# Kernel tuning notes

Measured on AMD Instinct MI355X. Metric: run time of the kernel, lower is better.

## Reference

```python
import jax, jax.numpy as jnp
import numpy as np

COST_CLASS, COST_BBOX, COST_GIOU = 1.0, 5.0, 2.0


def box_cxcywh_to_xyxy(x):
    cx, cy, w, h = x[..., 0], x[..., 1], x[..., 2], x[..., 3]
    return jnp.stack([cx - 0.5 * w, cy - 0.5 * h, cx + 0.5 * w, cy + 0.5 * h], axis=-1)


def generalized_box_iou(boxes1, boxes2):
    # boxes1: [M,4] xyxy, boxes2: [T,4] xyxy -> [M,T]
    area1 = (boxes1[:, 2] - boxes1[:, 0]) * (boxes1[:, 3] - boxes1[:, 1])
    area2 = (boxes2[:, 2] - boxes2[:, 0]) * (boxes2[:, 3] - boxes2[:, 1])
    lt = jnp.maximum(boxes1[:, None, :2], boxes2[None, :, :2])
    rb = jnp.minimum(boxes1[:, None, 2:], boxes2[None, :, 2:])
    wh = jnp.clip(rb - lt, 0.0)
    inter = wh[:, :, 0] * wh[:, :, 1]
    union = area1[:, None] + area2[None, :] - inter
    iou = inter / union
    lt_e = jnp.minimum(boxes1[:, None, :2], boxes2[None, :, :2])
    rb_e = jnp.maximum(boxes1[:, None, 2:], boxes2[None, :, 2:])
    wh_e = jnp.clip(rb_e - lt_e, 0.0)
    area = wh_e[:, :, 0] * wh_e[:, :, 1]
    return iou - (area - union) / area


def setup_inputs() -> dict:
    key = jax.random.key(0)
    k1, k2, k3, k4 = jax.random.split(key, 4)
    B, Q, C, T = 32, 900, 92, 2048
    pred_logits = jax.random.normal(k1, (B, Q, C), dtype=jnp.float32)
    pred_boxes = jax.random.uniform(k2, (B, Q, 4), dtype=jnp.float32, minval=0.05, maxval=0.95)
    tgt_labels = jax.random.randint(k3, (T,), 0, C)
    tgt_boxes = jax.random.uniform(k4, (T, 4), dtype=jnp.float32, minval=0.05, maxval=0.95)
    return {"pred_logits": pred_logits, "pred_boxes": pred_boxes,
            "tgt_labels": tgt_labels, "tgt_boxes": tgt_boxes}


def reference(pred_logits, pred_boxes, tgt_labels, tgt_boxes):
    B, Q, C = pred_logits.shape
    out_prob = jax.nn.softmax(pred_logits.reshape(B * Q, C), axis=-1)  # [BQ, C]
    out_bbox = pred_boxes.reshape(B * Q, 4)                            # [BQ, 4]
    cost_class = -out_prob[:, tgt_labels]                              # [BQ, T] gather
    cost_bbox = jnp.sum(jnp.abs(out_bbox[:, None, :] - tgt_boxes[None, :, :]), axis=-1)  # L1 cdist
    cost_giou = -generalized_box_iou(box_cxcywh_to_xyxy(out_bbox), box_cxcywh_to_xyxy(tgt_boxes))
    Cmat = COST_CLASS * cost_class + COST_BBOX * cost_bbox + COST_GIOU * cost_giou
    return Cmat.reshape(B, Q, -1)
```

## Files before the change

kernel.cpp:

```cpp
#include <hip/hip_runtime.h>
#include <math.h>

#define NCLS 92
#define NTGT 2048

__global__ __launch_bounds__(256) void matcher_cost_kernel(
    const float* __restrict__ logits,
    const float* __restrict__ pboxes,
    const int*   __restrict__ tlabels,
    const float* __restrict__ tboxes,
    float* __restrict__ out)
{
    const int row  = blockIdx.x;
    const int tid  = threadIdx.x;
    const int lane = tid & 63;

    __shared__ float s_prob[NCLS];

    const float* lrow = logits + (long)row * NCLS;
    float v0 = lrow[lane];
    float v1 = (lane + 64 < NCLS) ? lrow[lane + 64] : -INFINITY;
    float m = fmaxf(v0, v1);
    #pragma unroll
    for (int s = 32; s >= 1; s >>= 1) m = fmaxf(m, __shfl_xor(m, s, 64));
    float e0 = expf(v0 - m);
    float e1 = (lane + 64 < NCLS) ? expf(v1 - m) : 0.0f;
    float ssum = e0 + e1;
    #pragma unroll
    for (int s = 32; s >= 1; s >>= 1) ssum += __shfl_xor(ssum, s, 64);
    const float rs = 1.0f / ssum;
    if (tid < 64) {
        s_prob[lane] = e0 * rs;
        if (lane + 64 < NCLS) s_prob[lane + 64] = e1 * rs;
    }

    const float4 pb = *(const float4*)(pboxes + (long)row * 4);
    const float pcx = pb.x, pcy = pb.y, pw = pb.z, ph = pb.w;
    const float px0 = pcx - 0.5f * pw, py0 = pcy - 0.5f * ph;
    const float px1 = pcx + 0.5f * pw, py1 = pcy + 0.5f * ph;
    const float parea = (px1 - px0) * (py1 - py0);

    __syncthreads();

    float* orow = out + (long)row * NTGT;

    #pragma unroll
    for (int pass = 0; pass < 2; ++pass) {
        const int t = pass * 1024 + tid * 4;
        const int4 lab = *(const int4*)(tlabels + t);
        float c[4];
        #pragma unroll
        for (int j = 0; j < 4; ++j) {
            const float4 tb = *(const float4*)(tboxes + (long)(t + j) * 4);
            const float tcx = tb.x, tcy = tb.y, tw = tb.z, th = tb.w;
            const float tx0 = tcx - 0.5f * tw, ty0 = tcy - 0.5f * th;
            const float tx1 = tcx + 0.5f * tw, ty1 = tcy + 0.5f * th;
            const float tarea = (tx1 - tx0) * (ty1 - ty0);

            const int labj = (j == 0) ? lab.x : (j == 1) ? lab.y : (j == 2) ? lab.z : lab.w;
            const float cc = -s_prob[labj];

            const float cb = fabsf(pcx - tcx) + fabsf(pcy - tcy)
                           + fabsf(pw  - tw ) + fabsf(ph  - th );

            const float xl = fmaxf(px0, tx0), yt = fmaxf(py0, ty0);
            const float xr = fminf(px1, tx1), yb = fminf(py1, ty1);
            const float iw = fmaxf(xr - xl, 0.0f), ih = fmaxf(yb - yt, 0.0f);
            const float inter = iw * ih;
            const float uni = parea + tarea - inter;
            const float iou = __fdividef(inter, uni);
            const float ex0 = fminf(px0, tx0), ey0 = fminf(py0, ty0);
            const float ex1 = fmaxf(px1, tx1), ey1 = fmaxf(py1, ty1);
            const float ew = fmaxf(ex1 - ex0, 0.0f), eh = fmaxf(ey1 - ey0, 0.0f);
            const float earea = ew * eh;
            const float giou = iou - __fdividef(earea - uni, earea);

            c[j] = cc + 5.0f * cb - 2.0f * giou;
        }
        *(float4*)(orow + t) = make_float4(c[0], c[1], c[2], c[3]);
    }
}

extern "C" void kernel_launch(void* const* d_in, const int* in_sizes, int n_in,
                              void* d_out, int out_size, void* d_ws, size_t ws_size,
                              hipStream_t stream) {
    const float* logits  = (const float*)d_in[0];
    const float* pboxes  = (const float*)d_in[1];
    const int*   tlabels = (const int*)  d_in[2];
    const float* tboxes  = (const float*)d_in[3];
    float* out = (float*)d_out;

    const int BQ = in_sizes[1] / 4;
    matcher_cost_kernel<<<BQ, 256, 0, stream>>>(logits, pboxes, tlabels, tboxes, out);
}
```

Before: 302.7 us.

## Process sixteen query rows per block and reuse target boxes in registers

Each block now handles 16 prediction rows instead of one. Sixteen-lane groups compute the softmax for each row in parallel into shared memory. Target boxes and labels are loaded once per thread and reused across all rows, which cuts redundant global loads and per-block setup overhead. Output uses nontemporal vector stores to reduce cache pollution, and each thread keeps more values live in registers.

Result: no change. 298.6 us (-1.4%).

```diff
diff --git a/kernel.cpp b/kernel.cpp
--- a/kernel.cpp
+++ b/kernel.cpp
@@ -3,81 +3,118 @@
 
 #define NCLS 92
 #define NTGT 2048
+#define ROWS 16
+
+typedef float vfloat4 __attribute__((ext_vector_type(4)));
 
 __global__ __launch_bounds__(256) void matcher_cost_kernel(
     const float* __restrict__ logits,
     const float* __restrict__ pboxes,
     const int*   __restrict__ tlabels,
     const float* __restrict__ tboxes,
-    float* __restrict__ out)
+    float* __restrict__ out,
+    int BQ)
 {
-    const int row  = blockIdx.x;
+    const int row0 = blockIdx.x * ROWS;
     const int tid  = threadIdx.x;
-    const int lane = tid & 63;
+    const int rlim = min(ROWS, BQ - row0);
 
-    __shared__ float s_prob[NCLS];
+    __shared__ float s_prob[ROWS][NCLS + 1];
+    __shared__ float s_pb[ROWS][12];
 
-    const float* lrow = logits + (long)row * NCLS;
-    float v0 = lrow[lane];
-    float v1 = (lane + 64 < NCLS) ? lrow[lane + 64] : -INFINITY;
-    float m = fmaxf(v0, v1);
-    #pragma unroll
-    for (int s = 32; s >= 1; s >>= 1) m = fmaxf(m, __shfl_xor(m, s, 64));
-    float e0 = expf(v0 - m);
-    float e1 = (lane + 64 < NCLS) ? expf(v1 - m) : 0.0f;
-    float ssum = e0 + e1;
-    #pragma unroll
-    for (int s = 32; s >= 1; s >>= 1) ssum += __shfl_xor(ssum, s, 64);
-    const float rs = 1.0f / ssum;
-    if (tid < 64) {
-        s_prob[lane] = e0 * rs;
-        if (lane + 64 < NCLS) s_prob[lane + 64] = e1 * rs;
+    {
+        const int g = tid >> 4;
+        const int l = tid & 15;
+        const int gr = (g < rlim) ? g : 0;
+        const float* lrow = logits + (long)(row0 + gr) * NCLS;
+        float v[6];
+        float m = -INFINITY;
+        #pragma unroll
+        for (int k = 0; k < 6; ++k) {
+            const int c = l + k * 16;
+            v[k] = (c < NCLS) ? lrow[c] : -INFINITY;
+            m = fmaxf(m, v[k]);
+        }
+        #pragma unroll
+        for (int s = 8; s >= 1; s >>= 1) m = fmaxf(m, __shfl_xor(m, s, 16));
+        float sum = 0.0f;
+        #pragma unroll
+        for (int k = 0; k < 6; ++k) {
+            const int c = l + k * 16;
+            v[k] = (c < NCLS) ? expf(v[k] - m) : 0.0f;
+            sum += v[k];
+        }
+        #pragma unroll
+        for (int s = 8; s >= 1; s >>= 1) sum += __shfl_xor(sum, s, 16);
+        const float rs = 1.0f / sum;
+        #pragma unroll
+        for (int k = 0; k < 6; ++k) {
+            const int c = l + k * 16;
+            if (c < NCLS) s_prob[g][c] = v[k] * rs;
+        }
     }
-
-    const float4 pb = *(const float4*)(pboxes + (long)row * 4);
-    const float pcx = pb.x, pcy = pb.y, pw = pb.z, ph = pb.w;
-    const float px0 = pcx - 0.5f * pw, py0 = pcy - 0.5f * ph;
-    const float px1 = pcx + 0.5f * pw, py1 = pcy + 0.5f * ph;
-    const float parea = (px1 - px0) * (py1 - py0);
-
+    if (tid < ROWS) {
+        const int r = (tid < rlim) ? tid : 0;
+        const float4 pb = *(const float4*)(pboxes + (long)(row0 + r) * 4);
+        const float px0 = pb.x - 0.5f * pb.z, py0 = pb.y - 0.5f * pb.w;
+        const float px1 = pb.x + 0.5f * pb.z, py1 = pb.y + 0.5f * pb.w;
+        *(float4*)&s_pb[tid][0] = make_float4(px0, py0, px1, py1);
+        *(float4*)&s_pb[tid][4] = make_float4((px1 - px0) * (py1 - py0), pb.x, pb.y, pb.z);
+        s_pb[tid][8] = pb.w;
+    }
     __syncthreads();
 
-    float* orow = out + (long)row * NTGT;
+    float* oblk = out + (long)row0 * NTGT;
 
     #pragma unroll
     for (int pass = 0; pass < 2; ++pass) {
         const int t = pass * 1024 + tid * 4;
         const int4 lab = *(const int4*)(tlabels + t);
-        float c[4];
+        const int labs[4] = {lab.x, lab.y, lab.z, lab.w};
+
+        float tx0[4], ty0[4], tx1[4], ty1[4], tarea[4], tcx[4], tcy[4], tw[4], th[4];
         #pragma unroll
         for (int j = 0; j < 4; ++j) {
             const float4 tb = *(const float4*)(tboxes + (long)(t + j) * 4);
-            const float tcx = tb.x, tcy = tb.y, tw = tb.z, th = tb.w;
-            const float tx0 = tcx - 0.5f * tw, ty0 = tcy - 0.5f * th;
-            const float tx1 = tcx + 0.5f * tw, ty1 = tcy + 0.5f * th;
-            const float tarea = (tx1 - tx0) * (ty1 - ty0);
+            tcx[j] = tb.x; tcy[j] = tb.y; tw[j] = tb.z; th[j] = tb.w;
+            tx0[j] = tb.x - 0.5f * tb.z; ty0[j] = tb.y - 0.5f * tb.w;
+            tx1[j] = tb.x + 0.5f * tb.z; ty1[j] = tb.y + 0.5f * tb.w;
+            tarea[j] = (tx1[j] - tx0[j]) * (ty1[j] - ty0[j]);
+        }
 
-            const int labj = (j == 0) ? lab.x : (j == 1) ? lab.y : (j == 2) ? lab.z : lab.w;
-            const float cc = -s_prob[labj];
+        #pragma unroll 2
+        for (int r = 0; r < ROWS; ++r) {
+            if (r >= rlim) break;
+            const float4 p0 = *(const float4*)&s_pb[r][0];
+            const float4 p1 = *(const float4*)&s_pb[r][4];
+            const float  ph = s_pb[r][8];
+            float c[4];
+            #pragma unroll
+            for (int j = 0; j < 4; ++j) {
+                const float cc = -s_prob[r][labs[j]];
 
-            const float cb = fabsf(pcx - tcx) + fabsf(pcy - tcy)
-                           + fabsf(pw  - tw ) + fabsf(ph  - th );
+                const float cb = fabsf(p1.y - tcx[j]) + fabsf(p1.z - tcy[j])
+                               + fabsf(p1.w - tw[j]) + fabsf(ph - th[j]);
 
-            const float xl = fmaxf(px0, tx0), yt = fmaxf(py0, ty0);
-            const float xr = fminf(px1, tx1), yb = fminf(py1, ty1);
-            const float iw = fmaxf(xr - xl, 0.0f), ih = fmaxf(yb - yt, 0.0f);
-            const float inter = iw * ih;
-            const float uni = parea + tarea - inter;
-            const float iou = __fdividef(inter, uni);
-            const float ex0 = fminf(px0, tx0), ey0 = fminf(py0, ty0);
-            const float ex1 = fmaxf(px1, tx1), ey1 = fmaxf(py1, ty1);
-            const float ew = fmaxf(ex1 - ex0, 0.0f), eh = fmaxf(ey1 - ey0, 0.0f);
-            const float earea = ew * eh;
-            const float giou = iou - __fdividef(earea - uni, earea);
+                const float xl = fmaxf(p0.x, tx0[j]), yt = fmaxf(p0.y, ty0[j]);
+                const float xr = fminf(p0.z, tx1[j]), yb = fminf(p0.w, ty1[j]);
+                const float iw = fmaxf(xr - xl, 0.0f), ih = fmaxf(yb - yt, 0.0f);
+                const float inter = iw * ih;
+                const float uni = p1.x + tarea[j] - inter;
+                const float iou = __fdividef(inter, uni);
 
-            c[j] = cc + 5.0f * cb - 2.0f * giou;
+                const float ex0 = fminf(p0.x, tx0[j]), ey0 = fminf(p0.y, ty0[j]);
+                const float ex1 = fmaxf(p0.z, tx1[j]), ey1 = fmaxf(p0.w, ty1[j]);
+                const float ew = fmaxf(ex1 - ex0, 0.0f), eh = fmaxf(ey1 - ey0, 0.0f);
+                const float earea = ew * eh;
+                const float giou = iou - __fdividef(earea - uni, earea);
+
+                c[j] = cc + 5.0f * cb - 2.0f * giou;
+            }
+            vfloat4 cv;
+            cv.x = c[0]; cv.y = c[1]; cv.z = c[2]; cv.w = c[3];
+            __builtin_nontemporal_store(cv, (vfloat4*)(oblk + (long)r * NTGT + t));
         }
-        *(float4*)(orow + t) = make_float4(c[0], c[1], c[2], c[3]);
     }
 }
 
@@ -91,5 +128,6 @@
     float* out = (float*)d_out;
 
     const int BQ = in_sizes[1] / 4;
-    matcher_cost_kernel<<<BQ, 256, 0, stream>>>(logits, pboxes, tlabels, tboxes, out);
+    const int nblk = (BQ + ROWS - 1) / ROWS;
+    matcher_cost_kernel<<<nblk, 256, 0, stream>>>(logits, pboxes, tlabels, tboxes, out, BQ);
 }
```
